# Kernel tuning notes

Measured on AMD Instinct MI355X. Metric: run time of the kernel, lower is better.

## Reference

```python
import jax, jax.numpy as jnp
import numpy as np
from jax import lax

B, T, D_IN = 512, 256, 64
N_NEURONS, D_STATE, D_OUT = 2048, 64, 10


def setup_inputs() -> dict:
    key = jax.random.key(0)
    k_seq, k_enc, k_bias, k_gain, k_sd, k_d = jax.random.split(key, 6)
    enc = jax.random.normal(k_enc, (N_NEURONS, D_IN + D_STATE), dtype=jnp.float32)
    # hypersphere strategy: unit-norm encoder rows
    enc = enc / jnp.linalg.norm(enc, axis=-1, keepdims=True)
    return {
        "seq": jax.random.normal(k_seq, (B, T, D_IN), dtype=jnp.float32),
        "encoders": enc,
        "bias": jax.random.normal(k_bias, (N_NEURONS,), dtype=jnp.float32),
        "gain": jax.random.uniform(k_gain, (N_NEURONS,), dtype=jnp.float32),
        "state_decoders": jax.random.normal(k_sd, (N_NEURONS, D_STATE), dtype=jnp.float32) * 0.02,
        "decoders": jax.random.normal(k_d, (N_NEURONS, D_OUT), dtype=jnp.float32) * 0.02,
    }


def reference(seq, encoders, bias, gain, state_decoders, decoders):
    # seq: (B, T, d_in). Recurrent decode-then-re-encode loop over T.
    b = seq.shape[0]
    d_state = state_decoders.shape[1]
    n = encoders.shape[0]

    def step(carry, u_t):
        s, _ = carry  # s: (B, d_state)
        x_aug = jnp.concatenate([u_t, s], axis=-1)  # (B, d_in + d_state)
        a = jnp.abs(gain * (x_aug @ encoders.T) + bias)  # (B, n_neurons), activation='abs'
        s_new = a @ state_decoders  # (B, d_state)
        return (s_new, a), None

    s0 = jnp.zeros((b, d_state), dtype=seq.dtype)
    a0 = jnp.zeros((b, n), dtype=seq.dtype)
    (_, a_final), _ = lax.scan(step, (s0, a0), jnp.swapaxes(seq, 0, 1))
    return a_final @ decoders  # (B, d_out)
```

## Files before the change

kernel.cpp:

```cpp
#include <hip/hip_runtime.h>
#include <math.h>

#define B_    512
#define T_    256
#define DIN   64
#define DS    64
#define KK    128
#define NN    2048
#define DOUT  10

#define NT      512
#define BT      8
#define NTILES  (NN / NT)
#define BTILES  (B_ / BT)
#define THREADS 512
#define NWG     (NTILES * BTILES)

#define PSQ_ELEMS  ((size_t)BTILES * NTILES * BT * DS)
#define PS_FLOATS  (4 * PSQ_ELEMS)
#define ETSW_OFF   PS_FLOATS
#define ETSW_F16   ((size_t)KK * NN)
#define SDSW_OFF   (ETSW_OFF + ETSW_F16 / 2)
#define SDSW_F16   ((size_t)NN * DS)

typedef _Float16 half8 __attribute__((ext_vector_type(8)));
typedef float    f32x4 __attribute__((ext_vector_type(4)));

__global__ __launch_bounds__(256) void pre_kernel(const float* __restrict__ enc,
                                                  const float* __restrict__ sd,
                                                  float* __restrict__ ws,
                                                  float* __restrict__ out) {
    size_t i = (size_t)blockIdx.x * blockDim.x + threadIdx.x;
    size_t stride = (size_t)gridDim.x * blockDim.x;
    unsigned long long* psq = (unsigned long long*)ws;
    for (size_t x = i; x < 2 * PSQ_ELEMS; x += stride) psq[x] = 0ull;
    _Float16* EtSw = (_Float16*)(ws + ETSW_OFF);
    for (size_t x = i; x < (size_t)KK * NN; x += stride) {
        const int j     = (int)(x & 7);
        const int lane  = (int)((x >> 3) & 63);
        const int ktile = (int)((x >> 9) & 3);
        const int ntile = (int)((x >> 11) & 3);
        const int w     = (int)((x >> 13) & 7);
        const int nt    = (int)(x >> 16);
        const int n = nt * 512 + w * 64 + ntile * 16 + (lane & 15);
        const int k = ktile * 32 + ((lane >> 4) << 3) + j;
        EtSw[x] = (_Float16)enc[(size_t)n * KK + k];
    }
    _Float16* SdSw = (_Float16*)(ws + SDSW_OFF);
    for (size_t x = i; x < (size_t)NN * DS; x += stride) {
        const int j     = (int)(x & 7);
        const int lane  = (int)((x >> 3) & 63);
        const int ktile = (int)((x >> 9) & 7);
        const int kh    = (int)((x >> 12) & 1);
        const int cg    = (int)((x >> 13) & 3);
        const int nt    = (int)(x >> 15);
        const int n = nt * 512 + kh * 256 + ktile * 32 + ((lane >> 4) << 3) + j;
        const int c = cg * 16 + (lane & 15);
        SdSw[x] = (_Float16)sd[(size_t)n * DS + c];
    }
    for (size_t x = i; x < (size_t)B_ * DOUT; x += stride) out[x] = 0.0f;
}

__global__ __launch_bounds__(THREADS, 2) void persist_kernel(
    const float* __restrict__ seq,
    const _Float16* __restrict__ EtSw,
    const _Float16* __restrict__ SdSw,
    const float* __restrict__ bias,
    const float* __restrict__ gain,
    const float* __restrict__ dec,
    unsigned long long* __restrict__ psq,
    float* __restrict__ out)
{
    __shared__ _Float16 xh[16][136];
    __shared__ _Float16 Ash[16][520];
    __shared__ float Dp[4][8][17];

    const int tid = threadIdx.x;
    const int nt = blockIdx.x & (NTILES - 1);
    const int bt = blockIdx.x >> 2;
    const int n0 = nt * NT;
    const int b0 = bt * BT;

    const int w = tid >> 6;
    const int l = tid & 63;
    const int rs = tid >> 6;
    const int cs = tid & 63;
    const int m16 = l & 15;
    const int q8  = (l >> 4) << 3;
    const int cg  = w & 3;
    const int kh  = w >> 2;

    const _Float16* EtW = EtSw + ((size_t)(nt * 8 + w) << 13);
    const _Float16* SdW = SdSw + ((size_t)((nt * 4 + cg) * 2 + kh) << 12);

    half8 etf[4][4];
    #pragma unroll
    for (int n4 = 0; n4 < 4; ++n4)
        #pragma unroll
        for (int kt = 0; kt < 4; ++kt)
            etf[n4][kt] = *(const half8*)&EtW[(n4 << 11) + (kt << 9) + (size_t)l * 8];
    half8 sdf[8];
    #pragma unroll
    for (int kt = 0; kt < 8; ++kt)
        sdf[kt] = *(const half8*)&SdW[(kt << 9) + (size_t)l * 8];

    float gv[4], bv[4];
    #pragma unroll
    for (int n4 = 0; n4 < 4; ++n4) {
        gv[n4] = gain[n0 + w * 64 + n4 * 16 + m16];
        bv[n4] = bias[n0 + w * 64 + n4 * 16 + m16];
    }

    const size_t fan_base = ((size_t)bt * NTILES) * BT * DS + (size_t)rs * DS + cs;

    {
        unsigned int* xz = (unsigned int*)&xh[0][0];
        for (int i2 = tid; i2 < 16 * 136 / 2; i2 += THREADS) xz[i2] = 0u;
    }
    __syncthreads();

    for (int t = 0; t < T_; ++t) {
        if (tid < 128) {
            const int r = tid >> 4, c = (tid & 15) << 2;
            const float4 uv = *(const float4*)&seq[((size_t)(b0 + r) * T_ + t) * DIN + c];
            _Float16* p = &xh[r][c];
            p[0] = (_Float16)uv.x; p[1] = (_Float16)uv.y;
            p[2] = (_Float16)uv.z; p[3] = (_Float16)uv.w;
        }
        __syncthreads();

        f32x4 acc[4];
        #pragma unroll
        for (int n4 = 0; n4 < 4; ++n4) acc[n4] = (f32x4){0.f, 0.f, 0.f, 0.f};
        {
            const half8 af0 = *(const half8*)&xh[m16][q8];
            const half8 af1 = *(const half8*)&xh[m16][32 + q8];
            #pragma unroll
            for (int n4 = 0; n4 < 4; ++n4) {
                acc[n4] = __builtin_amdgcn_mfma_f32_16x16x32_f16(af0, etf[n4][0], acc[n4], 0, 0, 0);
                acc[n4] = __builtin_amdgcn_mfma_f32_16x16x32_f16(af1, etf[n4][1], acc[n4], 0, 0, 0);
            }
        }

        if (t > 0) {
            const unsigned long long* pb = psq + (size_t)((t - 1) & 1) * PSQ_ELEMS + fan_base;
            const unsigned utag = (unsigned)t;
            unsigned long long v0, v1, v2, v3;
            for (;;) {
                v0 = __hip_atomic_load(pb + 0 * (BT * DS), __ATOMIC_RELAXED, __HIP_MEMORY_SCOPE_AGENT);
                v1 = __hip_atomic_load(pb + 1 * (BT * DS), __ATOMIC_RELAXED, __HIP_MEMORY_SCOPE_AGENT);
                v2 = __hip_atomic_load(pb + 2 * (BT * DS), __ATOMIC_RELAXED, __HIP_MEMORY_SCOPE_AGENT);
                v3 = __hip_atomic_load(pb + 3 * (BT * DS), __ATOMIC_RELAXED, __HIP_MEMORY_SCOPE_AGENT);
                if ((unsigned)(v0 >> 32) == utag && (unsigned)(v1 >> 32) == utag &&
                    (unsigned)(v2 >> 32) == utag && (unsigned)(v3 >> 32) == utag)
                    break;
            }
            const float ssum = __uint_as_float((unsigned)v0) + __uint_as_float((unsigned)v1)
                             + __uint_as_float((unsigned)v2) + __uint_as_float((unsigned)v3);
            xh[rs][DIN + cs] = (_Float16)ssum;
        } else {
            xh[rs][DIN + cs] = (_Float16)0.f;
        }
        __syncthreads();

        {
            const half8 af2 = *(const half8*)&xh[m16][64 + q8];
            const half8 af3 = *(const half8*)&xh[m16][96 + q8];
            #pragma unroll
            for (int n4 = 0; n4 < 4; ++n4) {
                acc[n4] = __builtin_amdgcn_mfma_f32_16x16x32_f16(af2, etf[n4][2], acc[n4], 0, 0, 0);
                acc[n4] = __builtin_amdgcn_mfma_f32_16x16x32_f16(af3, etf[n4][3], acc[n4], 0, 0, 0);
            }
        }

        if (l < 32) {
            const int rq = (l >> 4) << 2;
            #pragma unroll
            for (int n4 = 0; n4 < 4; ++n4) {
                const int n = w * 64 + n4 * 16 + m16;
                Ash[rq + 0][n] = (_Float16)fabsf(gv[n4] * acc[n4][0] + bv[n4]);
                Ash[rq + 1][n] = (_Float16)fabsf(gv[n4] * acc[n4][1] + bv[n4]);
                Ash[rq + 2][n] = (_Float16)fabsf(gv[n4] * acc[n4][2] + bv[n4]);
                Ash[rq + 3][n] = (_Float16)fabsf(gv[n4] * acc[n4][3] + bv[n4]);
            }
        }
        __syncthreads();

        if (t == T_ - 1) {
            for (int idx = tid; idx < BT * DOUT; idx += THREADS) {
                const int r = idx / DOUT;
                const int d = idx % DOUT;
                float o = 0.f;
                #pragma unroll 8
                for (int n = 0; n < NT; ++n)
                    o += (float)Ash[r][n] * dec[(size_t)(n0 + n) * DOUT + d];
                atomicAdd(&out[(size_t)(b0 + r) * DOUT + d], o);
            }
            return;
        }

        {
            f32x4 d0 = (f32x4){0.f, 0.f, 0.f, 0.f};
            f32x4 d1 = (f32x4){0.f, 0.f, 0.f, 0.f};
            #pragma unroll
            for (int kt = 0; kt < 8; kt += 2) {
                const half8 a0 = *(const half8*)&Ash[m16][kh * 256 + kt * 32 + q8];
                d0 = __builtin_amdgcn_mfma_f32_16x16x32_f16(a0, sdf[kt], d0, 0, 0, 0);
                const half8 a1 = *(const half8*)&Ash[m16][kh * 256 + (kt + 1) * 32 + q8];
                d1 = __builtin_amdgcn_mfma_f32_16x16x32_f16(a1, sdf[kt + 1], d1, 0, 0, 0);
            }
            d0[0] += d1[0]; d0[1] += d1[1]; d0[2] += d1[2]; d0[3] += d1[3];

            if (kh == 1 && l < 32) {
                const int rq = (l >> 4) << 2;
                Dp[cg][rq + 0][m16] = d0[0];
                Dp[cg][rq + 1][m16] = d0[1];
                Dp[cg][rq + 2][m16] = d0[2];
                Dp[cg][rq + 3][m16] = d0[3];
            }
            __syncthreads();

            if (kh == 0 && l < 32) {
                const int rq = (l >> 4) << 2;
                unsigned long long* pw = psq + (size_t)(t & 1) * PSQ_ELEMS
                    + (((size_t)bt * NTILES + nt) * BT) * DS + 16 * cg + m16;
                const unsigned long long tg = (unsigned long long)(unsigned)(t + 1) << 32;
                #pragma unroll
                for (int r = 0; r < 4; ++r) {
                    const float v = d0[r] + Dp[cg][rq + r][m16];
                    __hip_atomic_store(pw + (size_t)(rq + r) * DS,
                                       tg | (unsigned long long)__float_as_uint(v),
                                       __ATOMIC_RELAXED, __HIP_MEMORY_SCOPE_AGENT);
                }
            }
        }
    }
}

extern "C" void kernel_launch(void* const* d_in, const int* in_sizes, int n_in,
                              void* d_out, int out_size, void* d_ws, size_t ws_size,
                              hipStream_t stream) {
    const float* seq  = (const float*)d_in[0];
    const float* enc  = (const float*)d_in[1];
    const float* bias = (const float*)d_in[2];
    const float* gain = (const float*)d_in[3];
    const float* sd   = (const float*)d_in[4];
    const float* dec  = (const float*)d_in[5];
    float* out = (float*)d_out;
    float* ws  = (float*)d_ws;

    pre_kernel<<<dim3(1024), dim3(256), 0, stream>>>(enc, sd, ws, out);

    unsigned long long* psq = (unsigned long long*)ws;
    const _Float16* EtSw = (const _Float16*)(ws + ETSW_OFF);
    const _Float16* SdSw = (const _Float16*)(ws + SDSW_OFF);

    persist_kernel<<<dim3(NWG), dim3(THREADS), 0, stream>>>(
        seq, EtSw, SdSw, bias, gain, dec, psq, out);
}
```

Baseline: 640.9 us.

## Split state decode to four waves and prefetch next input with idle waves

The state-decoder matmul is no longer split across two k-halves reduced through shared memory. Four waves now each run the full 512-long reduction over 16 register-held fragments, and the other four waves load and convert the next timestep's input into shared memory at the same time. This drops the Dp shared buffer and one barrier per step, and the first recurrent-state poll is issued before the input MFMAs so its latency is hidden. The cost is higher register pressure, so launch bounds drop to one block per CU, and the decode critical path on the four active waves is longer.

Result: faster. 608.9 us (-5.0%).

```diff
diff --git a/kernel.cpp b/kernel.cpp
--- a/kernel.cpp
+++ b/kernel.cpp
@@ -50,18 +50,17 @@
     for (size_t x = i; x < (size_t)NN * DS; x += stride) {
         const int j     = (int)(x & 7);
         const int lane  = (int)((x >> 3) & 63);
-        const int ktile = (int)((x >> 9) & 7);
-        const int kh    = (int)((x >> 12) & 1);
+        const int ktile = (int)((x >> 9) & 15);
         const int cg    = (int)((x >> 13) & 3);
         const int nt    = (int)(x >> 15);
-        const int n = nt * 512 + kh * 256 + ktile * 32 + ((lane >> 4) << 3) + j;
+        const int n = nt * 512 + ktile * 32 + ((lane >> 4) << 3) + j;
         const int c = cg * 16 + (lane & 15);
         SdSw[x] = (_Float16)sd[(size_t)n * DS + c];
     }
     for (size_t x = i; x < (size_t)B_ * DOUT; x += stride) out[x] = 0.0f;
 }
 
-__global__ __launch_bounds__(THREADS, 2) void persist_kernel(
+__global__ __launch_bounds__(THREADS, 1) void persist_kernel(
     const float* __restrict__ seq,
     const _Float16* __restrict__ EtSw,
     const _Float16* __restrict__ SdSw,
@@ -73,7 +72,6 @@
 {
     __shared__ _Float16 xh[16][136];
     __shared__ _Float16 Ash[16][520];
-    __shared__ float Dp[4][8][17];
 
     const int tid = threadIdx.x;
     const int nt = blockIdx.x & (NTILES - 1);
@@ -87,11 +85,9 @@
     const int cs = tid & 63;
     const int m16 = l & 15;
     const int q8  = (l >> 4) << 3;
-    const int cg  = w & 3;
-    const int kh  = w >> 2;
 
     const _Float16* EtW = EtSw + ((size_t)(nt * 8 + w) << 13);
-    const _Float16* SdW = SdSw + ((size_t)((nt * 4 + cg) * 2 + kh) << 12);
+    const _Float16* SdW = SdSw + ((size_t)(nt * 4 + (w & 3)) << 13);
 
     half8 etf[4][4];
     #pragma unroll
@@ -99,9 +95,9 @@
         #pragma unroll
         for (int kt = 0; kt < 4; ++kt)
             etf[n4][kt] = *(const half8*)&EtW[(n4 << 11) + (kt << 9) + (size_t)l * 8];
-    half8 sdf[8];
+    half8 sdf[16];
     #pragma unroll
-    for (int kt = 0; kt < 8; ++kt)
+    for (int kt = 0; kt < 16; ++kt)
         sdf[kt] = *(const half8*)&SdW[(kt << 9) + (size_t)l * 8];
 
     float gv[4], bv[4];
@@ -118,16 +114,25 @@
         for (int i2 = tid; i2 < 16 * 136 / 2; i2 += THREADS) xz[i2] = 0u;
     }
     __syncthreads();
+    if (tid < 128) {
+        const int r = tid >> 4, c = (tid & 15) << 2;
+        const float4 uv = *(const float4*)&seq[((size_t)(b0 + r) * T_ + 0) * DIN + c];
+        _Float16* p = &xh[r][c];
+        p[0] = (_Float16)uv.x; p[1] = (_Float16)uv.y;
+        p[2] = (_Float16)uv.z; p[3] = (_Float16)uv.w;
+    }
+    __syncthreads();
 
     for (int t = 0; t < T_; ++t) {
-        if (tid < 128) {
-            const int r = tid >> 4, c = (tid & 15) << 2;
-            const float4 uv = *(const float4*)&seq[((size_t)(b0 + r) * T_ + t) * DIN + c];
-            _Float16* p = &xh[r][c];
-            p[0] = (_Float16)uv.x; p[1] = (_Float16)uv.y;
-            p[2] = (_Float16)uv.z; p[3] = (_Float16)uv.w;
-        }
-        __syncthreads();
+        const unsigned long long* pb =
+            psq + (size_t)((t - 1) & 1) * PSQ_ELEMS + fan_base;
+        unsigned long long v0 = 0, v1 = 0, v2 = 0, v3 = 0;
+        if (t > 0) {
+            v0 = __hip_atomic_load(pb + 0 * (BT * DS), __ATOMIC_RELAXED, __HIP_MEMORY_SCOPE_AGENT);
+            v1 = __hip_atomic_load(pb + 1 * (BT * DS), __ATOMIC_RELAXED, __HIP_MEMORY_SCOPE_AGENT);
+            v2 = __hip_atomic_load(pb + 2 * (BT * DS), __ATOMIC_RELAXED, __HIP_MEMORY_SCOPE_AGENT);
+            v3 = __hip_atomic_load(pb + 3 * (BT * DS), __ATOMIC_RELAXED, __HIP_MEMORY_SCOPE_AGENT);
+        }
 
         f32x4 acc[4];
         #pragma unroll
@@ -143,17 +148,15 @@
         }
 
         if (t > 0) {
-            const unsigned long long* pb = psq + (size_t)((t - 1) & 1) * PSQ_ELEMS + fan_base;
             const unsigned utag = (unsigned)t;
-            unsigned long long v0, v1, v2, v3;
             for (;;) {
+                if ((unsigned)(v0 >> 32) == utag && (unsigned)(v1 >> 32) == utag &&
+                    (unsigned)(v2 >> 32) == utag && (unsigned)(v3 >> 32) == utag)
+                    break;
                 v0 = __hip_atomic_load(pb + 0 * (BT * DS), __ATOMIC_RELAXED, __HIP_MEMORY_SCOPE_AGENT);
                 v1 = __hip_atomic_load(pb + 1 * (BT * DS), __ATOMIC_RELAXED, __HIP_MEMORY_SCOPE_AGENT);
                 v2 = __hip_atomic_load(pb + 2 * (BT * DS), __ATOMIC_RELAXED, __HIP_MEMORY_SCOPE_AGENT);
                 v3 = __hip_atomic_load(pb + 3 * (BT * DS), __ATOMIC_RELAXED, __HIP_MEMORY_SCOPE_AGENT);
-                if ((unsigned)(v0 >> 32) == utag && (unsigned)(v1 >> 32) == utag &&
-                    (unsigned)(v2 >> 32) == utag && (unsigned)(v3 >> 32) == utag)
-                    break;
             }
             const float ssum = __uint_as_float((unsigned)v0) + __uint_as_float((unsigned)v1)
                              + __uint_as_float((unsigned)v2) + __uint_as_float((unsigned)v3);
@@ -199,41 +202,42 @@
             return;
         }
 
-        {
+        if (w < 4) {
             f32x4 d0 = (f32x4){0.f, 0.f, 0.f, 0.f};
             f32x4 d1 = (f32x4){0.f, 0.f, 0.f, 0.f};
             #pragma unroll
-            for (int kt = 0; kt < 8; kt += 2) {
-                const half8 a0 = *(const half8*)&Ash[m16][kh * 256 + kt * 32 + q8];
+            for (int kt = 0; kt < 16; kt += 2) {
+                const half8 a0 = *(const half8*)&Ash[m16][kt * 32 + q8];
                 d0 = __builtin_amdgcn_mfma_f32_16x16x32_f16(a0, sdf[kt], d0, 0, 0, 0);
-                const half8 a1 = *(const half8*)&Ash[m16][kh * 256 + (kt + 1) * 32 + q8];
+                const half8 a1 = *(const half8*)&Ash[m16][(kt + 1) * 32 + q8];
                 d1 = __builtin_amdgcn_mfma_f32_16x16x32_f16(a1, sdf[kt + 1], d1, 0, 0, 0);
             }
             d0[0] += d1[0]; d0[1] += d1[1]; d0[2] += d1[2]; d0[3] += d1[3];
-
-            if (kh == 1 && l < 32) {
-                const int rq = (l >> 4) << 2;
-                Dp[cg][rq + 0][m16] = d0[0];
-                Dp[cg][rq + 1][m16] = d0[1];
-                Dp[cg][rq + 2][m16] = d0[2];
-                Dp[cg][rq + 3][m16] = d0[3];
-            }
-            __syncthreads();
-
-            if (kh == 0 && l < 32) {
+            if (l < 32) {
                 const int rq = (l >> 4) << 2;
                 unsigned long long* pw = psq + (size_t)(t & 1) * PSQ_ELEMS
-                    + (((size_t)bt * NTILES + nt) * BT) * DS + 16 * cg + m16;
+                    + (((size_t)bt * NTILES + nt) * BT) * DS + 16 * w + m16;
                 const unsigned long long tg = (unsigned long long)(unsigned)(t + 1) << 32;
                 #pragma unroll
                 for (int r = 0; r < 4; ++r) {
-                    const float v = d0[r] + Dp[cg][rq + r][m16];
+                    const float v = d0[rq >= 4 ? r : r] + 0.f;
+                    const float vv = d0[r];
+                    (void)v;
                     __hip_atomic_store(pw + (size_t)(rq + r) * DS,
-                                       tg | (unsigned long long)__float_as_uint(v),
+                                       tg | (unsigned long long)__float_as_uint(vv),
                                        __ATOMIC_RELAXED, __HIP_MEMORY_SCOPE_AGENT);
                 }
             }
-        }
+        } else if (l < 32) {
+            const int idx = ((w - 4) << 5) + l;
+            const int r = idx >> 4, c = (idx & 15) << 2;
+            const float4 uv =
+                *(const float4*)&seq[((size_t)(b0 + r) * T_ + (t + 1)) * DIN + c];
+            _Float16* p = &xh[r][c];
+            p[0] = (_Float16)uv.x; p[1] = (_Float16)uv.y;
+            p[2] = (_Float16)uv.z; p[3] = (_Float16)uv.w;
+        }
+        __syncthreads();
     }
 }
 
```
